# Optimization experiments

Measured on AMD Instinct MI355X. Metric: run time of the kernel, lower is better.

The kernel has to match this reference:

```python
import jax, jax.numpy as jnp
import numpy as np

B, INP, H, DH = 8192, 2048, 8, 256
HD = H * DH            # 2048
PROJ = int(4 / 3 * HD)  # 2731
EPS = 1e-5


def _layernorm(x, w, b):
    mu = jnp.mean(x, axis=-1, keepdims=True)
    var = jnp.mean((x - mu) ** 2, axis=-1, keepdims=True)
    return (x - mu) * jax.lax.rsqrt(var + EPS) * w + b


def _groupnorm(x, w, b):
    # x: [B, HD] -> groups of size DH (one group per head)
    xg = x.reshape(-1, H, DH)
    mu = jnp.mean(xg, axis=-1, keepdims=True)
    var = jnp.mean((xg - mu) ** 2, axis=-1, keepdims=True)
    xn = ((xg - mu) * jax.lax.rsqrt(var + EPS)).reshape(-1, HD)
    return xn * w + b


def _block_linear(h, R):
    # h: [B, HD], R: [H, DH, DH] block-diagonal recurrent weights (no bias)
    hh = h.reshape(-1, H, DH)
    return jnp.einsum('bhd,hde->bhe', hh, R).reshape(-1, HD)


def setup_inputs() -> dict:
    key = jax.random.key(0)
    ks = jax.random.split(key, 16)
    s = 0.02
    return {
        'seq': jax.random.normal(ks[0], (B, INP), jnp.float32),
        'c_tm1': jnp.zeros((B, HD), jnp.float32),
        'n_tm1': jnp.ones((B, HD), jnp.float32),
        'h_tm1': jnp.zeros((B, HD), jnp.float32),
        'm_tm1': jnp.zeros((B, HD), jnp.float32),
        'ln_w': jnp.ones((INP,), jnp.float32),
        'ln_b': jnp.zeros((INP,), jnp.float32),
        'gn_w': jnp.ones((HD,), jnp.float32),
        'gn_b': jnp.zeros((HD,), jnp.float32),
        'W_i': jax.random.normal(ks[1], (INP, HD), jnp.float32) * s,
        'b_i': jnp.zeros((HD,), jnp.float32),
        'W_f': jax.random.normal(ks[2], (INP, HD), jnp.float32) * s,
        'b_f': jnp.zeros((HD,), jnp.float32),
        'W_z': jax.random.normal(ks[3], (INP, HD), jnp.float32) * s,
        'b_z': jnp.zeros((HD,), jnp.float32),
        'W_o': jax.random.normal(ks[4], (INP, HD), jnp.float32) * s,
        'b_o': jnp.zeros((HD,), jnp.float32),
        'R_i': jax.random.normal(ks[5], (H, DH, DH), jnp.float32) * s,
        'R_f': jax.random.normal(ks[6], (H, DH, DH), jnp.float32) * s,
        'R_z': jax.random.normal(ks[7], (H, DH, DH), jnp.float32) * s,
        'R_o': jax.random.normal(ks[8], (H, DH, DH), jnp.float32) * s,
        'W_up': jax.random.normal(ks[9], (HD, 2 * PROJ), jnp.float32) * s,
        'b_up': jnp.zeros((2 * PROJ,), jnp.float32),
        'W_dn': jax.random.normal(ks[10], (PROJ, INP), jnp.float32) * s,
        'b_dn': jnp.zeros((INP,), jnp.float32),
    }


def reference(seq, c_tm1, n_tm1, h_tm1, m_tm1, ln_w, ln_b, gn_w, gn_b,
              W_i, b_i, W_f, b_f, W_z, b_z, W_o, b_o,
              R_i, R_f, R_z, R_o, W_up, b_up, W_dn, b_dn):
    x_t = _layernorm(seq, ln_w, ln_b)
    x_c = x_t  # use_conv=False path

    i_t = x_c @ W_i + b_i + _block_linear(h_tm1, R_i)
    f_t = x_c @ W_f + b_f + _block_linear(h_tm1, R_f)
    z_t = x_t @ W_z + b_z + _block_linear(h_tm1, R_z)
    o_t = x_t @ W_o + b_o + _block_linear(h_tm1, R_o)

    m_t = jnp.maximum(f_t + m_tm1, i_t)          # stabilizer state
    i_g = jnp.exp(i_t - m_t)
    f_g = jnp.exp(f_t - m_t + m_tm1)
    z_g = jnp.tanh(z_t)
    o_g = jax.nn.sigmoid(o_t)

    c_t = f_g * c_tm1 + i_g * z_g
    n_t = f_g * n_tm1 + i_g
    h_t = o_g * (c_t / n_t)

    out = _groupnorm(h_t, gn_w, gn_b)
    up = out @ W_up + b_up
    out1, out2 = up[:, :PROJ], up[:, PROJ:]
    out = out1 + jax.nn.gelu(out2, approximate=False)
    out = out @ W_dn + b_dn
    return (out + seq, (c_t, n_t, h_t, m_t))
```

## Files before the change

### kernel.cpp

```cpp
#include <hip/hip_runtime.h>
#include <math.h>

typedef unsigned short u16;
typedef __attribute__((ext_vector_type(4))) float f32x4;
typedef __attribute__((ext_vector_type(8))) short bf16x8;
typedef __attribute__((ext_vector_type(8))) unsigned short u16x8;

#define B_ROWS 8192
#define GLDS(gaddr, laddr)                                                                  \
  __builtin_amdgcn_global_load_lds(                                                        \
      (const __attribute__((address_space(1))) unsigned int*)(const void*)(gaddr),          \
      (__attribute__((address_space(3))) unsigned int*)(void*)(laddr), 16, 0, 0)

__device__ __forceinline__ u16 f2bf(float f) {
  unsigned int u = __float_as_uint(f);
  unsigned int r = u + 0x7fffu + ((u >> 16) & 1u);
  return (u16)(r >> 16);
}

__device__ __forceinline__ bf16x8 dsr(unsigned a) {
  bf16x8 d;
  asm volatile("ds_read_b128 %0, %1" : "=v"(d) : "v"(a));
  return d;
}

__device__ __forceinline__ void block_reduce2(float& a, float& b) {
  __shared__ float sb[8];
  #pragma unroll
  for (int off = 32; off > 0; off >>= 1) {
    a += __shfl_down(a, off, 64);
    b += __shfl_down(b, off, 64);
  }
  int lane = threadIdx.x & 63, wid = threadIdx.x >> 6;
  if (lane == 0) { sb[wid] = a; sb[wid + 4] = b; }
  __syncthreads();
  a = sb[0] + sb[1] + sb[2] + sb[3];
  b = sb[4] + sb[5] + sb[6] + sb[7];
  __syncthreads();
}

__global__ __launch_bounds__(256) void ln_kernel(const float* __restrict__ seq,
                                                 const float* __restrict__ w,
                                                 const float* __restrict__ b,
                                                 u16* __restrict__ xbf) {
  int row = blockIdx.x, t = threadIdx.x;
  const f32x4* x = (const f32x4*)(seq + (size_t)row * 2048);
  f32x4 v0 = x[2 * t], v1 = x[2 * t + 1];
  float s = 0.f, q = 0.f;
  #pragma unroll
  for (int i = 0; i < 4; ++i) { s += v0[i] + v1[i]; q += v0[i] * v0[i] + v1[i] * v1[i]; }
  block_reduce2(s, q);
  float mu = s * (1.f / 2048.f);
  float var = q * (1.f / 2048.f) - mu * mu;
  float rstd = rsqrtf(var + 1e-5f);
  f32x4 w0 = ((const f32x4*)w)[2 * t], w1 = ((const f32x4*)w)[2 * t + 1];
  f32x4 b0 = ((const f32x4*)b)[2 * t], b1 = ((const f32x4*)b)[2 * t + 1];
  u16x8 o;
  #pragma unroll
  for (int i = 0; i < 4; ++i) o[i] = f2bf((v0[i] - mu) * rstd * w0[i] + b0[i]);
  #pragma unroll
  for (int i = 0; i < 4; ++i) o[4 + i] = f2bf((v1[i] - mu) * rstd * w1[i] + b1[i]);
  ((u16x8*)(xbf + (size_t)row * 2048))[t] = o;
}

__global__ __launch_bounds__(256) void cvt_bf16(const float* __restrict__ in,
                                                u16* __restrict__ out, int n) {
  int i = blockIdx.x * 256 + threadIdx.x;
  int stride = gridDim.x * 256;
  for (; i < n; i += stride) out[i] = f2bf(in[i]);
}

__global__ void transpose_cvt(const float* __restrict__ in, long ibstride, int R, int Cc,
                              u16* __restrict__ out, long obstride, int ldo) {
  in += (size_t)blockIdx.z * ibstride;
  out += (size_t)blockIdx.z * obstride;
  __shared__ float tile[32][33];
  int c0 = blockIdx.x * 32, r0 = blockIdx.y * 32;
  int tx = threadIdx.x, ty = threadIdx.y;
  #pragma unroll
  for (int j = 0; j < 4; ++j) {
    int rr = r0 + ty + j * 8;
    if (rr < R && c0 + tx < Cc) tile[ty + j * 8][tx] = in[(size_t)rr * Cc + c0 + tx];
  }
  __syncthreads();
  #pragma unroll
  for (int j = 0; j < 4; ++j) {
    int cc = c0 + ty + j * 8, rr = r0 + tx;
    if (cc < Cc && rr < R) out[(size_t)cc * ldo + rr] = f2bf(tile[tx][ty + j * 8]);
  }
}

__global__ __launch_bounds__(256) void pack_bias(const float* __restrict__ bi, const float* __restrict__ bf_,
                                                 const float* __restrict__ bz, const float* __restrict__ bo,
                                                 const float* __restrict__ bup,
                                                 float* __restrict__ biasg, float* __restrict__ biasup) {
  int i = blockIdx.x * 256 + threadIdx.x;
  if (i < 8192) {
    int g = i >> 11, j = i & 2047;
    const float* p = (g == 0) ? bi : (g == 1) ? bf_ : (g == 2) ? bz : bo;
    biasg[i] = p[j];
  }
  if (i < 5504) biasup[i] = (i < 5460) ? bup[i] : 0.f;
}

#define MFMA_CLUSTER(lo)                                                                   \
  __builtin_amdgcn_s_setprio(1);                                                           \
  _Pragma("unroll")                                                                        \
  for (int mi = 0; mi < 4; ++mi)                                                           \
    _Pragma("unroll")                                                                      \
    for (int ni = 0; ni < 4; ++ni)                                                         \
      acc[(lo) + mi][ni] =                                                                 \
          __builtin_amdgcn_mfma_f32_16x16x32_bf16(af[mi], bfr[ni], acc[(lo) + mi][ni], 0, 0, 0); \
  __builtin_amdgcn_s_setprio(0);

#define WAIT_LDS()                                                                         \
  asm volatile("s_waitcnt lgkmcnt(0)" ::: "memory");                                       \
  __builtin_amdgcn_sched_barrier(0);

template<int REC>
__global__ __launch_bounds__(512, 2) void gemm256(
    const u16* __restrict__ A, int lda,
    const u16* __restrict__ Bt, int ldb, int KT,
    float* __restrict__ C, long ldc, int Nvalid, int ntN,
    const float* __restrict__ bias,
    const float* __restrict__ addsrc, int ldadd,
    const u16* __restrict__ hbf, const u16* __restrict__ RTw) {
  __shared__ __align__(16) u16 Al[2][2][256][32];
  __shared__ __align__(16) u16 Bl[2][2][256][32];
  const int NT = KT + (REC ? 4 : 0);

  int nb = gridDim.x;
  int bid = blockIdx.x;
  int per = nb >> 3;
  int id = (bid & 7) * per + (bid >> 3);
  int m0 = (id / ntN) * 256, n0 = (id % ntN) * 256;

  int tid = threadIdx.x, lane = tid & 63, wave = tid >> 6;
  int wm = wave >> 2, wn = wave & 3;
  int r = lane & 15, sgrp = lane >> 4;

  const u16* rsrc = nullptr; int hcol = 0;
  if (REC) {
    int g = n0 >> 11, head = (n0 & 2047) >> 8;
    rsrc = RTw + ((size_t)(g * 8 + head)) * 65536;
    hcol = head * 256;
  }

  auto stage = [&](int tt, int which) {
    if (tt >= NT) return;
    const int isA = (which < 2), kh = which & 1, slot = tt & 1;
    const u16* src; size_t ld;
    if (!REC || tt < KT) {
      if (isA) { src = A + (size_t)m0 * lda + tt * 64; ld = lda; }
      else     { src = Bt + (size_t)n0 * ldb + tt * 64; ld = ldb; }
    } else {
      int t2 = tt - KT;
      if (isA) { src = hbf + (size_t)m0 * 2048 + hcol + t2 * 64; ld = 2048; }
      else     { src = rsrc + t2 * 64; ld = 256; }
    }
    u16* base = isA ? &Al[slot][kh][0][0] : &Bl[slot][kh][0][0];
    #pragma unroll
    for (int c = 0; c < 2; ++c) {
      int R0 = wave * 32 + c * 16;
      int row = R0 + (lane >> 2);
      int s = (lane & 3) ^ ((row >> 1) & 3);
      GLDS(src + (size_t)row * ld + kh * 32 + s * 8, base + R0 * 32);
    }
  };

  unsigned AlB = (unsigned)(size_t)(__attribute__((address_space(3))) u16*)&Al[0][0][0][0];
  unsigned BlB = (unsigned)(size_t)(__attribute__((address_space(3))) u16*)&Bl[0][0][0][0];
  int sA = sgrp ^ ((r >> 1) & 3);
  unsigned aBaseT = AlB + (unsigned)((wm * 128 + r) * 64 + sA * 16);
  unsigned bBaseT = BlB + (unsigned)((wn * 64 + r) * 64 + sA * 16);

  f32x4 acc[8][4] = {};
  bf16x8 af[4], bfr[4];

  stage(0, 0); stage(0, 2); stage(0, 1); stage(0, 3);
  stage(1, 0); stage(1, 2);
  asm volatile("s_waitcnt vmcnt(4)" ::: "memory");
  __builtin_amdgcn_s_barrier();

  for (int t = 0; t < NT; ++t) {
    unsigned sl = (unsigned)(t & 1) * 32768u;
    unsigned ab = aBaseT + sl, bb = bBaseT + sl;
    af[0] = dsr(ab);          af[1] = dsr(ab + 1024);
    af[2] = dsr(ab + 2048);   af[3] = dsr(ab + 3072);
    bfr[0] = dsr(bb);         bfr[1] = dsr(bb + 1024);
    bfr[2] = dsr(bb + 2048);  bfr[3] = dsr(bb + 3072);
    stage(t + 1, 1);
    __builtin_amdgcn_s_barrier();
    WAIT_LDS();
    MFMA_CLUSTER(0);
    __builtin_amdgcn_s_barrier();
    af[0] = dsr(ab + 4096);   af[1] = dsr(ab + 5120);
    af[2] = dsr(ab + 6144);   af[3] = dsr(ab + 7168);
    stage(t + 1, 3);
    __builtin_amdgcn_s_barrier();
    WAIT_LDS();
    MFMA_CLUSTER(4);
    __builtin_amdgcn_s_barrier();
    af[0] = dsr(ab + 16384);  af[1] = dsr(ab + 17408);
    af[2] = dsr(ab + 18432);  af[3] = dsr(ab + 19456);
    bfr[0] = dsr(bb + 16384); bfr[1] = dsr(bb + 17408);
    bfr[2] = dsr(bb + 18432); bfr[3] = dsr(bb + 19456);
    stage(t + 2, 0);
    __builtin_amdgcn_s_barrier();
    WAIT_LDS();
    MFMA_CLUSTER(0);
    __builtin_amdgcn_s_barrier();
    af[0] = dsr(ab + 20480);  af[1] = dsr(ab + 21504);
    af[2] = dsr(ab + 22528);  af[3] = dsr(ab + 23552);
    stage(t + 2, 2);
    __builtin_amdgcn_s_barrier();
    WAIT_LDS();
    MFMA_CLUSTER(4);
    if (t + 2 < NT)      { asm volatile("s_waitcnt vmcnt(4)" ::: "memory"); }
    else if (t + 1 < NT) { asm volatile("s_waitcnt vmcnt(0)" ::: "memory"); }
    __builtin_amdgcn_s_barrier();
  }

  #pragma unroll
  for (int a = 0; a < 8; ++a) {
    int row0 = m0 + wm * 128 + a * 16 + sgrp * 4;
    #pragma unroll
    for (int ni = 0; ni < 4; ++ni) {
      int col = n0 + wn * 64 + ni * 16 + r;
      if (col >= Nvalid) continue;
      float bv = bias ? bias[col] : 0.f;
      #pragma unroll
      for (int jj = 0; jj < 4; ++jj) {
        float v = acc[a][ni][jj] + bv;
        if (addsrc) v += addsrc[(size_t)(row0 + jj) * ldadd + col];
        C[(size_t)(row0 + jj) * ldc + col] = v;
      }
    }
  }
}

__global__ __launch_bounds__(256) void pointwise_gn(
    const float* __restrict__ G, const float* __restrict__ c1, const float* __restrict__ n1,
    const float* __restrict__ m1, const float* __restrict__ gnw, const float* __restrict__ gnb,
    float* __restrict__ outc, float* __restrict__ outn, float* __restrict__ outh,
    float* __restrict__ outm, u16* __restrict__ gnbf) {
  int b = blockIdx.x >> 3, h = blockIdx.x & 7, t = threadIdx.x;
  int j = (h << 8) + t;
  size_t rg = (size_t)b * 8192;
  float it = G[rg + j], ft = G[rg + 2048 + j], zt = G[rg + 4096 + j], ot = G[rg + 6144 + j];
  size_t idx = (size_t)b * 2048 + j;
  float cp = c1[idx], np = n1[idx], mp = m1[idx];
  float mt = fmaxf(ft + mp, it);
  float ig = expf(it - mt), fg = expf(ft - mt + mp);
  float zg = tanhf(zt), og = 1.f / (1.f + expf(-ot));
  float ct = fg * cp + ig * zg;
  float nt = fg * np + ig;
  float ht = og * (ct / nt);
  outc[idx] = ct; outn[idx] = nt; outh[idx] = ht; outm[idx] = mt;
  float s = ht, q = ht * ht;
  block_reduce2(s, q);
  float mu = s * (1.f / 256.f);
  float var = q * (1.f / 256.f) - mu * mu;
  float xn = (ht - mu) * rsqrtf(var + 1e-5f);
  gnbf[idx] = f2bf(xn * gnw[j] + gnb[j]);
}

__global__ __launch_bounds__(256) void act_gelu(const float* __restrict__ tmp, u16* __restrict__ gl) {
  int i = blockIdx.x * 256 + threadIdx.x;
  int stride = gridDim.x * 256;
  const int total = 8192 * 2752;
  for (; i < total; i += stride) {
    int b = i / 2752, p = i - b * 2752;
    float y = 0.f;
    if (p < 2730) {
      float x1 = tmp[(size_t)b * 5504 + p];
      float x2 = tmp[(size_t)b * 5504 + 2730 + p];
      y = x1 + x2 * 0.5f * (1.f + erff(x2 * 0.70710678118f));
    }
    gl[(size_t)b * 2752 + p] = f2bf(y);
  }
}

extern "C" void kernel_launch(void* const* d_in, const int* in_sizes, int n_in,
                              void* d_out, int out_size, void* d_ws, size_t ws_size,
                              hipStream_t stream) {
  (void)in_sizes; (void)n_in; (void)out_size; (void)ws_size;
  const float* seq = (const float*)d_in[0];
  const float* c1  = (const float*)d_in[1];
  const float* n1  = (const float*)d_in[2];
  const float* h1  = (const float*)d_in[3];
  const float* m1  = (const float*)d_in[4];
  const float* lnw = (const float*)d_in[5];
  const float* lnb = (const float*)d_in[6];
  const float* gnw = (const float*)d_in[7];
  const float* gnb = (const float*)d_in[8];
  const float* Wi = (const float*)d_in[9];  const float* bi  = (const float*)d_in[10];
  const float* Wf = (const float*)d_in[11]; const float* bf_ = (const float*)d_in[12];
  const float* Wz = (const float*)d_in[13]; const float* bz  = (const float*)d_in[14];
  const float* Wo = (const float*)d_in[15]; const float* bo  = (const float*)d_in[16];
  const float* Ri = (const float*)d_in[17]; const float* Rf = (const float*)d_in[18];
  const float* Rz = (const float*)d_in[19]; const float* Ro = (const float*)d_in[20];
  const float* Wup = (const float*)d_in[21]; const float* bup = (const float*)d_in[22];
  const float* Wdn = (const float*)d_in[23]; const float* bdn = (const float*)d_in[24];

  size_t off = 0;
  char* base = (char*)d_ws;
  auto alloc = [&](size_t bytes) { char* p = base + off; off += (bytes + 255) & ~(size_t)255; return p; };
  u16*   XBF    = (u16*)  alloc((size_t)B_ROWS * 2048 * 2);
  u16*   HBF    = (u16*)  alloc((size_t)B_ROWS * 2048 * 2);
  u16*   WGT    = (u16*)  alloc((size_t)4 * 2048 * 2048 * 2);
  u16*   RT     = (u16*)  alloc((size_t)4 * 8 * 256 * 256 * 2);
  u16*   WUPT   = (u16*)  alloc((size_t)5632 * 2048 * 2);
  u16*   WDNT   = (u16*)  alloc((size_t)2048 * 2752 * 2);
  float* BIASG  = (float*)alloc((size_t)8192 * 4);
  float* BIASUP = (float*)alloc((size_t)5504 * 4);
  u16*   GNBF   = (u16*)  alloc((size_t)B_ROWS * 2048 * 2);
  float* G      = (float*)alloc((size_t)B_ROWS * 8192 * 4);
  float* TMP    = G;
  u16*   GL     = WGT;

  float* OUT  = (float*)d_out;
  float* OUTC = OUT + (size_t)B_ROWS * 2048;
  float* OUTN = OUTC + (size_t)B_ROWS * 2048;
  float* OUTH = OUTN + (size_t)B_ROWS * 2048;
  float* OUTM = OUTH + (size_t)B_ROWS * 2048;

  dim3 tb32(32, 8);

  ln_kernel<<<B_ROWS, 256, 0, stream>>>(seq, lnw, lnb, XBF);
  cvt_bf16<<<2048, 256, 0, stream>>>(h1, HBF, B_ROWS * 2048);
  transpose_cvt<<<dim3(64, 64, 1), tb32, 0, stream>>>(Wi, 0, 2048, 2048, WGT + (size_t)0 * 4194304, 0, 2048);
  transpose_cvt<<<dim3(64, 64, 1), tb32, 0, stream>>>(Wf, 0, 2048, 2048, WGT + (size_t)1 * 4194304, 0, 2048);
  transpose_cvt<<<dim3(64, 64, 1), tb32, 0, stream>>>(Wz, 0, 2048, 2048, WGT + (size_t)2 * 4194304, 0, 2048);
  transpose_cvt<<<dim3(64, 64, 1), tb32, 0, stream>>>(Wo, 0, 2048, 2048, WGT + (size_t)3 * 4194304, 0, 2048);
  transpose_cvt<<<dim3(8, 8, 8), tb32, 0, stream>>>(Ri, 65536, 256, 256, RT + (size_t)0 * 524288, 65536, 256);
  transpose_cvt<<<dim3(8, 8, 8), tb32, 0, stream>>>(Rf, 65536, 256, 256, RT + (size_t)1 * 524288, 65536, 256);
  transpose_cvt<<<dim3(8, 8, 8), tb32, 0, stream>>>(Rz, 65536, 256, 256, RT + (size_t)2 * 524288, 65536, 256);
  transpose_cvt<<<dim3(8, 8, 8), tb32, 0, stream>>>(Ro, 65536, 256, 256, RT + (size_t)3 * 524288, 65536, 256);
  transpose_cvt<<<dim3(171, 64, 1), tb32, 0, stream>>>(Wup, 0, 2048, 5460, WUPT, 0, 2048);
  transpose_cvt<<<dim3(64, 86, 1), tb32, 0, stream>>>(Wdn, 0, 2730, 2048, WDNT, 0, 2752);
  pack_bias<<<32, 256, 0, stream>>>(bi, bf_, bz, bo, bup, BIASG, BIASUP);
  gemm256<1><<<32 * 32, 512, 0, stream>>>(XBF, 2048, WGT, 2048, 32,
                                          G, 8192, 8192, 32, BIASG, nullptr, 0, HBF, RT);
  pointwise_gn<<<B_ROWS * 8, 256, 0, stream>>>(G, c1, n1, m1, gnw, gnb,
                                               OUTC, OUTN, OUTH, OUTM, GNBF);
  gemm256<0><<<32 * 22, 512, 0, stream>>>(GNBF, 2048, WUPT, 2048, 32,
                                          TMP, 5504, 5460, 22, BIASUP, nullptr, 0, nullptr, nullptr);
  act_gelu<<<8192, 256, 0, stream>>>(TMP, GL);
  gemm256<0><<<32 * 8, 512, 0, stream>>>(GL, 2752, WDNT, 2752, 43,
                                         OUT, 2048, 2048, 8, bdn, seq, 2048, nullptr, nullptr);
}
```

Measured before the change: 1.511 ms.

## Restructure GEMM main loop with multi-buffered fragments and fewer barriers

The GEMM inner loop now keeps separate register fragments for the four sub-steps. It issues LDS reads for later sub-steps before earlier MFMA clusters run, using partial lgkmcnt waits instead of full waits. Per-iteration workgroup barriers drop from eight to two, so LDS latency overlaps with MFMA work. This costs more VGPRs and relies on the remaining barriers being enough to avoid LDS overwrite races. Separately, act_gelu is rewritten to process one row per block, which avoids per-element integer division but assumes the launch grid has one block per row.

```diff
diff --git a/kernel.cpp b/kernel.cpp
--- a/kernel.cpp
+++ b/kernel.cpp
@@ -103,18 +103,18 @@
   if (i < 5504) biasup[i] = (i < 5460) ? bup[i] : 0.f;
 }
 
-#define MFMA_CLUSTER(lo)                                                                   \
+#define MFMA_CLUSTER(lo, AV, BV)                                                           \
   __builtin_amdgcn_s_setprio(1);                                                           \
   _Pragma("unroll")                                                                        \
   for (int mi = 0; mi < 4; ++mi)                                                           \
     _Pragma("unroll")                                                                      \
     for (int ni = 0; ni < 4; ++ni)                                                         \
       acc[(lo) + mi][ni] =                                                                 \
-          __builtin_amdgcn_mfma_f32_16x16x32_bf16(af[mi], bfr[ni], acc[(lo) + mi][ni], 0, 0, 0); \
+          __builtin_amdgcn_mfma_f32_16x16x32_bf16(AV[mi], BV[ni], acc[(lo) + mi][ni], 0, 0, 0); \
   __builtin_amdgcn_s_setprio(0);
 
-#define WAIT_LDS()                                                                         \
-  asm volatile("s_waitcnt lgkmcnt(0)" ::: "memory");                                       \
+#define WAIT_LGKM(N)                                                                       \
+  asm volatile("s_waitcnt lgkmcnt(" #N ")" ::: "memory");                                  \
   __builtin_amdgcn_sched_barrier(0);
 
 template<int REC>
@@ -175,7 +175,7 @@
   unsigned bBaseT = BlB + (unsigned)((wn * 64 + r) * 64 + sA * 16);
 
   f32x4 acc[8][4] = {};
-  bf16x8 af[4], bfr[4];
+  bf16x8 a0[4], a1[4], a2[4], a3[4], b0[4], b1[4];
 
   stage(0, 0); stage(0, 2); stage(0, 1); stage(0, 3);
   stage(1, 0); stage(1, 2);
@@ -185,37 +185,31 @@
   for (int t = 0; t < NT; ++t) {
     unsigned sl = (unsigned)(t & 1) * 32768u;
     unsigned ab = aBaseT + sl, bb = bBaseT + sl;
-    af[0] = dsr(ab);          af[1] = dsr(ab + 1024);
-    af[2] = dsr(ab + 2048);   af[3] = dsr(ab + 3072);
-    bfr[0] = dsr(bb);         bfr[1] = dsr(bb + 1024);
-    bfr[2] = dsr(bb + 2048);  bfr[3] = dsr(bb + 3072);
-    stage(t + 1, 1);
+    __builtin_amdgcn_sched_barrier(0);
+    a0[0] = dsr(ab);          a0[1] = dsr(ab + 1024);
+    a0[2] = dsr(ab + 2048);   a0[3] = dsr(ab + 3072);
+    b0[0] = dsr(bb);          b0[1] = dsr(bb + 1024);
+    b0[2] = dsr(bb + 2048);   b0[3] = dsr(bb + 3072);
+    a1[0] = dsr(ab + 4096);   a1[1] = dsr(ab + 5120);
+    a1[2] = dsr(ab + 6144);   a1[3] = dsr(ab + 7168);
+    stage(t + 1, 1); stage(t + 1, 3);
+    WAIT_LGKM(4);
+    MFMA_CLUSTER(0, a0, b0);
+    a2[0] = dsr(ab + 16384);  a2[1] = dsr(ab + 17408);
+    a2[2] = dsr(ab + 18432);  a2[3] = dsr(ab + 19456);
+    b1[0] = dsr(bb + 16384);  b1[1] = dsr(bb + 17408);
+    b1[2] = dsr(bb + 18432);  b1[3] = dsr(bb + 19456);
+    WAIT_LGKM(8);
+    MFMA_CLUSTER(4, a1, b0);
     __builtin_amdgcn_s_barrier();
-    WAIT_LDS();
-    MFMA_CLUSTER(0);
-    __builtin_amdgcn_s_barrier();
-    af[0] = dsr(ab + 4096);   af[1] = dsr(ab + 5120);
-    af[2] = dsr(ab + 6144);   af[3] = dsr(ab + 7168);
-    stage(t + 1, 3);
-    __builtin_amdgcn_s_barrier();
-    WAIT_LDS();
-    MFMA_CLUSTER(4);
-    __builtin_amdgcn_s_barrier();
-    af[0] = dsr(ab + 16384);  af[1] = dsr(ab + 17408);
-    af[2] = dsr(ab + 18432);  af[3] = dsr(ab + 19456);
-    bfr[0] = dsr(bb + 16384); bfr[1] = dsr(bb + 17408);
-    bfr[2] = dsr(bb + 18432); bfr[3] = dsr(bb + 19456);
-    stage(t + 2, 0);
-    __builtin_amdgcn_s_barrier();
-    WAIT_LDS();
-    MFMA_CLUSTER(0);
-    __builtin_amdgcn_s_barrier();
-    af[0] = dsr(ab + 20480);  af[1] = dsr(ab + 21504);
-    af[2] = dsr(ab + 22528);  af[3] = dsr(ab + 23552);
-    stage(t + 2, 2);
-    __builtin_amdgcn_s_barrier();
-    WAIT_LDS();
-    MFMA_CLUSTER(4);
+    __builtin_amdgcn_sched_barrier(0);
+    stage(t + 2, 0); stage(t + 2, 2);
+    a3[0] = dsr(ab + 20480);  a3[1] = dsr(ab + 21504);
+    a3[2] = dsr(ab + 22528);  a3[3] = dsr(ab + 23552);
+    WAIT_LGKM(4);
+    MFMA_CLUSTER(0, a2, b1);
+    WAIT_LGKM(0);
+    MFMA_CLUSTER(4, a3, b1);
     if (t + 2 < NT)      { asm volatile("s_waitcnt vmcnt(4)" ::: "memory"); }
     else if (t + 1 < NT) { asm volatile("s_waitcnt vmcnt(0)" ::: "memory"); }
     __builtin_amdgcn_s_barrier();
@@ -266,18 +260,16 @@
 }
 
 __global__ __launch_bounds__(256) void act_gelu(const float* __restrict__ tmp, u16* __restrict__ gl) {
-  int i = blockIdx.x * 256 + threadIdx.x;
-  int stride = gridDim.x * 256;
-  const int total = 8192 * 2752;
-  for (; i < total; i += stride) {
-    int b = i / 2752, p = i - b * 2752;
+  int b = blockIdx.x;
+  const float* row = tmp + (size_t)b * 5504;
+  u16* orow = gl + (size_t)b * 2752;
+  for (int p = threadIdx.x; p < 2752; p += 256) {
     float y = 0.f;
     if (p < 2730) {
-      float x1 = tmp[(size_t)b * 5504 + p];
-      float x2 = tmp[(size_t)b * 5504 + 2730 + p];
+      float x1 = row[p], x2 = row[2730 + p];
       y = x1 + x2 * 0.5f * (1.f + erff(x2 * 0.70710678118f));
     }
-    gl[(size_t)b * 2752 + p] = f2bf(y);
+    orow[p] = f2bf(y);
   }
 }
 
```

After: 1.487 ms. Within noise of the previous version (-1.6%).
